# Performance work log

Hardware: AMD Instinct MI355X
Metric: run time of the kernel (lower is better)

The kernel has to match this reference:

```python
import jax, jax.numpy as jnp
import numpy as np
import math

B, H, S, D = 2, 16, 2048, 64
MASK_NEG = -1e9


def setup_inputs() -> dict:
    key = jax.random.key(0)
    kq, kk, kv, kc, km = jax.random.split(key, 5)
    q = jax.random.normal(kq, (B, H, S, D), dtype=jnp.float32)
    k = jax.random.normal(kk, (B, H, S, D), dtype=jnp.float32)
    v = jax.random.normal(kv, (B, H, S, D), dtype=jnp.float32)
    constant = jax.random.normal(kc, (1, H, 1, 1), dtype=jnp.float32)
    mask = jax.random.randint(km, (B, S), 0, 2, dtype=jnp.int32)  # 1 = masked out
    return {"q": q, "k": k, "v": v, "constant": constant, "mask": mask}


def leaky_softmax(x, leaky_factor):
    # custom 'leaky' softmax: denominator gets an extra exp(c - max) * S term
    m = jnp.max(x, axis=-1, keepdims=True)
    exp_x = jnp.exp(x - m)
    leak = jnp.exp(leaky_factor - m) * x.shape[-1]
    return exp_x / (jnp.sum(exp_x, axis=-1, keepdims=True) + leak)


def reference(q, k, v, constant, mask):
    scale = jnp.float32(1.0 / math.sqrt(q.shape[-1]))
    # scores: [B,H,S,S]
    scores = jnp.einsum("bhqd,bhkd->bhqk", q, k) * scale
    m = mask.astype(q.dtype)[:, None, None, :]  # [B,1,1,S]
    scores = scores + m * MASK_NEG
    probs = leaky_softmax(scores, constant)
    out = jnp.einsum("bhqk,bhkd->bhqd", probs, v)
    return out, probs
```

## Files before the change

kernel.cpp:

```cpp
#include <hip/hip_runtime.h>
#include <hip/hip_bf16.h>
#include <cstdint>
#include <cstddef>

#define BB 2
#define HH 16
#define SS 2048
#define DD 64
#define NBH (BB * HH)
#define BQ 16
#define NWAVES 8
#define BLK 512
#define CW 512
#define NCHUNK (SS / CW)
#define CSTRIDE 516

typedef __attribute__((ext_vector_type(8))) short bf16x8;
typedef __attribute__((ext_vector_type(4))) float f32x4;
typedef __attribute__((ext_vector_type(4))) unsigned short us4;

#define LGKM_BAR() asm volatile("s_waitcnt lgkmcnt(0)\n\ts_barrier" ::: "memory")

__device__ __forceinline__ unsigned short f2bf(float x) {
  union { float f; uint32_t u; } c;
  c.f = x;
  uint32_t u = c.u;
  uint32_t r = (u + 0x7FFFu + ((u >> 16) & 1u)) >> 16;
  return (unsigned short)r;
}

__global__ __launch_bounds__(256) void cvt_qk_kernel(
    const float* __restrict__ q, const float* __restrict__ k,
    unsigned short* __restrict__ qb, unsigned short* __restrict__ kb) {
  size_t i = ((size_t)blockIdx.x * 256 + threadIdx.x) * 4;
  float4 a = *(const float4*)(q + i);
  float4 b = *(const float4*)(k + i);
  us4 qa = {f2bf(a.x), f2bf(a.y), f2bf(a.z), f2bf(a.w)};
  us4 ka = {f2bf(b.x), f2bf(b.y), f2bf(b.z), f2bf(b.w)};
  *(us4*)(qb + i) = qa;
  *(us4*)(kb + i) = ka;
}

__global__ __launch_bounds__(256) void cvt_vt_kernel(
    const float* __restrict__ v, unsigned short* __restrict__ vt) {
  __shared__ unsigned short t[64][65];
  const int tid = threadIdx.x;
  const int bh = blockIdx.y;
  const int s0 = blockIdx.x * 64;
  const float* vb = v + ((size_t)bh * SS + s0) * DD;
#pragma unroll
  for (int it = 0; it < 16; ++it) {
    int idx = it * 256 + tid;
    int s = idx >> 6, d = idx & 63;
    t[s][d] = f2bf(vb[idx]);
  }
  __syncthreads();
  unsigned short* vo = vt + (size_t)bh * DD * SS + s0;
#pragma unroll
  for (int it = 0; it < 16; ++it) {
    int idx = it * 256 + tid;
    int d = idx >> 6, s = idx & 63;
    vo[(size_t)d * SS + s] = t[s][d];
  }
}

__global__ __launch_bounds__(BLK, 2) void attn_kernel(
    const unsigned short* __restrict__ qb,
    const unsigned short* __restrict__ kb,
    const unsigned short* __restrict__ vt,
    const float* __restrict__ cst,
    const int* __restrict__ mask,
    float* __restrict__ out,
    float* __restrict__ probs) {
  __shared__ float pch[BQ][CSTRIDE];
  __shared__ float stats[NWAVES][BQ];
  __shared__ float rowinv[BQ];

  const int tid = threadIdx.x;
  const int wave = tid >> 6;
  const int lane = tid & 63;
  const int quad = lane >> 4;
  const int l16 = lane & 15;
  const int bh = blockIdx.y;
  const int bidx = bh >> 4;
  const int h = bh & 15;
  const int q0 = blockIdx.x * BQ;

  const unsigned short* qrow = qb + ((size_t)bh * SS + q0 + l16) * DD + quad * 8;
  bf16x8 aq0 = *(const bf16x8*)(qrow);
  bf16x8 aq1 = *(const bf16x8*)(qrow + 32);

  const unsigned short* kbase = kb + (size_t)bh * SS * DD;
  f32x4 acc[16];
#pragma unroll
  for (int t = 0; t < 16; ++t) {
    int col0 = (wave + 8 * t) * 16;
    const unsigned short* krow = kbase + (size_t)(col0 + l16) * DD + quad * 8;
    bf16x8 bk0 = *(const bf16x8*)(krow);
    bf16x8 bk1 = *(const bf16x8*)(krow + 32);
    f32x4 c = {0.f, 0.f, 0.f, 0.f};
    c = __builtin_amdgcn_mfma_f32_16x16x32_bf16(aq0, bk0, c, 0, 0, 0);
    c = __builtin_amdgcn_mfma_f32_16x16x32_bf16(aq1, bk1, c, 0, 0, 0);
    acc[t] = c;
  }

  float rsum[4] = {0.f, 0.f, 0.f, 0.f};
#pragma unroll
  for (int t = 0; t < 16; ++t) {
    int col = (wave + 8 * t) * 16 + l16;
    int mk = mask[bidx * SS + col];
#pragma unroll
    for (int r = 0; r < 4; ++r) {
      float e = mk ? 0.0f : __expf(acc[t][r] * 0.125f);
      acc[t][r] = e;
      rsum[r] += e;
    }
  }
#pragma unroll
  for (int off = 8; off >= 1; off >>= 1)
#pragma unroll
    for (int r = 0; r < 4; ++r)
      rsum[r] += __shfl_xor(rsum[r], off, 64);
  if (l16 == 0)
#pragma unroll
    for (int r = 0; r < 4; ++r) stats[wave][quad * 4 + r] = rsum[r];
  __syncthreads();
  if (tid < BQ) {
    float s = 0.f;
#pragma unroll
    for (int w = 0; w < NWAVES; ++w) s += stats[w][tid];
    float denom = s + __expf(cst[h]) * (float)SS;
    rowinv[tid] = 1.0f / denom;
  }
  __syncthreads();
  float inv[4];
#pragma unroll
  for (int r = 0; r < 4; ++r) inv[r] = rowinv[quad * 4 + r];

  f32x4 acco[4];
#pragma unroll
  for (int dt = 0; dt < 4; ++dt) acco[dt] = (f32x4){0.f, 0.f, 0.f, 0.f};
  const unsigned short* vbase = vt + (size_t)bh * DD * SS;
#pragma unroll
  for (int c = 0; c < NCHUNK; ++c) {
    if (c) LGKM_BAR();
#pragma unroll
    for (int tt = 0; tt < 4; ++tt) {
      int t = c * 4 + tt;
      int lcol = tt * 128 + wave * 16 + l16;
#pragma unroll
      for (int r = 0; r < 4; ++r)
        pch[quad * 4 + r][lcol] = acc[t][r] * inv[r];
    }
    LGKM_BAR();
#pragma unroll
    for (int i = 0; i < 4; ++i) {
      int f = i * BLK + tid;
      int row = f >> 7, c4 = f & 127;
      f32x4 val = *(const f32x4*)&pch[row][c4 * 4];
      f32x4* dst = (f32x4*)(probs + (size_t)bh * SS * SS +
                            (size_t)(q0 + row) * SS + c * CW) + c4;
      __builtin_nontemporal_store(val, dst);
    }
#pragma unroll
    for (int ks = 0; ks < 2; ++ks) {
      int k0 = wave * 64 + ks * 32;
      const f32x4* ap4 = (const f32x4*)&pch[l16][k0 + quad * 8];
      f32x4 p0 = ap4[0], p1 = ap4[1];
      union { bf16x8 v8; uint32_t u[4]; } apu;
      asm("v_cvt_pk_bf16_f32 %0, %1, %2" : "=v"(apu.u[0]) : "v"(p0.x), "v"(p0.y));
      asm("v_cvt_pk_bf16_f32 %0, %1, %2" : "=v"(apu.u[1]) : "v"(p0.z), "v"(p0.w));
      asm("v_cvt_pk_bf16_f32 %0, %1, %2" : "=v"(apu.u[2]) : "v"(p1.x), "v"(p1.y));
      asm("v_cvt_pk_bf16_f32 %0, %1, %2" : "=v"(apu.u[3]) : "v"(p1.z), "v"(p1.w));
      bf16x8 ap = apu.v8;
      int kg = c * CW + k0 + quad * 8;
#pragma unroll
      for (int dt = 0; dt < 4; ++dt) {
        const unsigned short* vrow = vbase + (size_t)(dt * 16 + l16) * SS + kg;
        bf16x8 bv = *(const bf16x8*)vrow;
        acco[dt] = __builtin_amdgcn_mfma_f32_16x16x32_bf16(ap, bv, acco[dt], 0, 0, 0);
      }
    }
  }

  LGKM_BAR();
  float* outp = &pch[0][0];
#pragma unroll
  for (int dt = 0; dt < 4; ++dt)
#pragma unroll
    for (int r = 0; r < 4; ++r)
      outp[((wave * BQ) + quad * 4 + r) * DD + dt * 16 + l16] = acco[dt][r];
  LGKM_BAR();
  for (int e = tid; e < BQ * DD; e += BLK) {
    int row = e >> 6, col = e & 63;
    float s = 0.f;
#pragma unroll
    for (int w = 0; w < NWAVES; ++w) s += outp[(w * BQ + row) * DD + col];
    out[((size_t)bh * SS + q0 + row) * DD + col] = s;
  }
}

extern "C" void kernel_launch(void* const* d_in, const int* in_sizes, int n_in,
                              void* d_out, int out_size, void* d_ws, size_t ws_size,
                              hipStream_t stream) {
  const float* q = (const float*)d_in[0];
  const float* k = (const float*)d_in[1];
  const float* v = (const float*)d_in[2];
  const float* cst = (const float*)d_in[3];
  const int* mask = (const int*)d_in[4];

  float* out = (float*)d_out;
  float* probs = out + (size_t)NBH * SS * DD;

  const size_t nelem = (size_t)NBH * SS * DD;
  unsigned short* qb = (unsigned short*)d_ws;
  unsigned short* kb = qb + nelem;
  unsigned short* vt = kb + nelem;

  cvt_qk_kernel<<<dim3((unsigned)(nelem / (256 * 4))), 256, 0, stream>>>(q, k, qb, kb);
  cvt_vt_kernel<<<dim3(SS / 64, NBH), 256, 0, stream>>>(v, vt);

  attn_kernel<<<dim3(SS / BQ, NBH), BLK, 0, stream>>>(qb, kb, vt, cst, mask, out, probs);
}
```

Baseline: 739.7 us.

## Prefetch V tiles before barrier, reorder probs store after PV MFMAs, vectorize V transpose

In the attention kernel, the V operand loads for each chunk are now issued before the LDS barrier, so global-load latency overlaps the probability writes to LDS. The PV MFMAs are reordered so the second half's V loads are issued before the first half's MFMAs. The probs writeback now follows the MFMAs and uses plain stores instead of nontemporal stores. The V transpose kernel writes 4-element vectors instead of scalar shorts. The main cost targeted is exposed V-load latency; the change adds register pressure and changes cache behaviour for the large probs write.

```diff
diff --git a/kernel.cpp b/kernel.cpp
--- a/kernel.cpp
+++ b/kernel.cpp
@@ -57,10 +57,12 @@
   __syncthreads();
   unsigned short* vo = vt + (size_t)bh * DD * SS + s0;
 #pragma unroll
-  for (int it = 0; it < 16; ++it) {
+  for (int it = 0; it < 4; ++it) {
     int idx = it * 256 + tid;
-    int d = idx >> 6, s = idx & 63;
-    vo[(size_t)d * SS + s] = t[s][d];
+    int d = idx >> 4;
+    int s4 = (idx & 15) * 4;
+    us4 w = {t[s4 + 0][d], t[s4 + 1][d], t[s4 + 2][d], t[s4 + 3][d]};
+    *(us4*)(vo + (size_t)d * SS + s4) = w;
   }
 }
 
@@ -143,6 +145,12 @@
   const unsigned short* vbase = vt + (size_t)bh * DD * SS;
 #pragma unroll
   for (int c = 0; c < NCHUNK; ++c) {
+    const int kg0 = c * CW + wave * 64 + quad * 8;
+    bf16x8 v0[4];
+#pragma unroll
+    for (int dt = 0; dt < 4; ++dt)
+      v0[dt] = *(const bf16x8*)(vbase + (size_t)(dt * 16 + l16) * SS + kg0);
+
     if (c) LGKM_BAR();
 #pragma unroll
     for (int tt = 0; tt < 4; ++tt) {
@@ -153,19 +161,9 @@
         pch[quad * 4 + r][lcol] = acc[t][r] * inv[r];
     }
     LGKM_BAR();
-#pragma unroll
-    for (int i = 0; i < 4; ++i) {
-      int f = i * BLK + tid;
-      int row = f >> 7, c4 = f & 127;
-      f32x4 val = *(const f32x4*)&pch[row][c4 * 4];
-      f32x4* dst = (f32x4*)(probs + (size_t)bh * SS * SS +
-                            (size_t)(q0 + row) * SS + c * CW) + c4;
-      __builtin_nontemporal_store(val, dst);
-    }
-#pragma unroll
-    for (int ks = 0; ks < 2; ++ks) {
-      int k0 = wave * 64 + ks * 32;
-      const f32x4* ap4 = (const f32x4*)&pch[l16][k0 + quad * 8];
+
+    {
+      const f32x4* ap4 = (const f32x4*)&pch[l16][wave * 64 + quad * 8];
       f32x4 p0 = ap4[0], p1 = ap4[1];
       union { bf16x8 v8; uint32_t u[4]; } apu;
       asm("v_cvt_pk_bf16_f32 %0, %1, %2" : "=v"(apu.u[0]) : "v"(p0.x), "v"(p0.y));
@@ -173,13 +171,35 @@
       asm("v_cvt_pk_bf16_f32 %0, %1, %2" : "=v"(apu.u[2]) : "v"(p1.x), "v"(p1.y));
       asm("v_cvt_pk_bf16_f32 %0, %1, %2" : "=v"(apu.u[3]) : "v"(p1.z), "v"(p1.w));
       bf16x8 ap = apu.v8;
-      int kg = c * CW + k0 + quad * 8;
-#pragma unroll
-      for (int dt = 0; dt < 4; ++dt) {
-        const unsigned short* vrow = vbase + (size_t)(dt * 16 + l16) * SS + kg;
-        bf16x8 bv = *(const bf16x8*)vrow;
-        acco[dt] = __builtin_amdgcn_mfma_f32_16x16x32_bf16(ap, bv, acco[dt], 0, 0, 0);
-      }
+      bf16x8 v1[4];
+#pragma unroll
+      for (int dt = 0; dt < 4; ++dt)
+        v1[dt] = *(const bf16x8*)(vbase + (size_t)(dt * 16 + l16) * SS + kg0 + 32);
+#pragma unroll
+      for (int dt = 0; dt < 4; ++dt)
+        acco[dt] = __builtin_amdgcn_mfma_f32_16x16x32_bf16(ap, v0[dt], acco[dt], 0, 0, 0);
+
+      const f32x4* bp4 = (const f32x4*)&pch[l16][wave * 64 + 32 + quad * 8];
+      f32x4 q0v = bp4[0], q1v = bp4[1];
+      union { bf16x8 v8; uint32_t u[4]; } bpu;
+      asm("v_cvt_pk_bf16_f32 %0, %1, %2" : "=v"(bpu.u[0]) : "v"(q0v.x), "v"(q0v.y));
+      asm("v_cvt_pk_bf16_f32 %0, %1, %2" : "=v"(bpu.u[1]) : "v"(q0v.z), "v"(q0v.w));
+      asm("v_cvt_pk_bf16_f32 %0, %1, %2" : "=v"(bpu.u[2]) : "v"(q1v.x), "v"(q1v.y));
+      asm("v_cvt_pk_bf16_f32 %0, %1, %2" : "=v"(bpu.u[3]) : "v"(q1v.z), "v"(q1v.w));
+      bf16x8 bp = bpu.v8;
+#pragma unroll
+      for (int dt = 0; dt < 4; ++dt)
+        acco[dt] = __builtin_amdgcn_mfma_f32_16x16x32_bf16(bp, v1[dt], acco[dt], 0, 0, 0);
+    }
+
+#pragma unroll
+    for (int i = 0; i < 4; ++i) {
+      int f = i * BLK + tid;
+      int row = f >> 7, c4 = f & 127;
+      f32x4 val = *(const f32x4*)&pch[row][c4 * 4];
+      f32x4* dst = (f32x4*)(probs + (size_t)bh * SS * SS +
+                            (size_t)(q0 + row) * SS + c * CW) + c4;
+      *dst = val;
     }
   }
 
```

After: 849.7 us. 14.9% more time.
